# Performance work log

Hardware: AMD Instinct MI355X
Metric: run time of the kernel (lower is better)

The kernel has to match this reference:

```python
import jax, jax.numpy as jnp
import numpy as np

BATCH = 256
B_TYPES = 32   # input capsule types
C_TYPES = 10   # output capsule types
H, W = 8, 8    # input spatial extent == kernel (output is 1x1)
POSE = 16      # capsule pose length (shape (16,1))
NUM_ITER = 3
EPS = 1e-8


def setup_inputs() -> dict:
    key = jax.random.key(0)
    k1, k2, k3 = jax.random.split(key, 3)
    input_caps_poses = jax.random.normal(k1, (BATCH, B_TYPES, H, W, POSE, 1), jnp.float32)
    input_caps_activations = jax.random.uniform(k2, (BATCH, B_TYPES, H, W), jnp.float32)
    # nn.init.normal_(std=0.1) on [B, kh, kw, C, os0, is0]
    weight = 0.1 * jax.random.normal(k3, (B_TYPES, H, W, C_TYPES, POSE, POSE), jnp.float32)
    # routing_bias initialized to 0.1: [C, oh, ow, os0, os1]
    routing_bias = jnp.full((C_TYPES, 1, 1, POSE, 1), 0.1, jnp.float32)
    return {
        "input_caps_poses": input_caps_poses,
        "input_caps_activations": input_caps_activations,
        "weight": weight,
        "routing_bias": routing_bias,
    }


def _squash(s):
    # Hinton squash: ||s||^2/(1+||s||^2) * s/||s||, norm over pose dims
    n2 = jnp.sum(s * s, axis=(-2, -1), keepdims=True)
    return (n2 / (1.0 + n2)) * s * jax.lax.rsqrt(n2 + EPS)


def reference(input_caps_poses, input_caps_activations, weight, routing_bias):
    b = input_caps_poses.shape[0]
    # votes[b,c,B,h,w,o,p] = sum_i W[B,h,w,c,o,i] * pose[b,B,h,w,i,p]
    votes = jnp.einsum('Bhwcoi,bBhwip->bcBhwop', weight, input_caps_poses)
    logits = jnp.zeros((b, C_TYPES, B_TYPES, H, W), votes.dtype)
    bias = routing_bias.reshape(1, C_TYPES, POSE, 1)
    v = None
    for it in range(NUM_ITER):
        # coupling coefficients: softmax over output capsule types
        c = jax.nn.softmax(logits, axis=1)                      # [b,C,B,h,w]
        # weighted sum of votes over all input capsules (B,h,w)
        s = jnp.einsum('bcBhw,bcBhwop->bcop', c, votes) + bias  # [b,C,16,1]
        v = _squash(s)
        if it < NUM_ITER - 1:
            # agreement: dot(vote, output pose)
            logits = logits + jnp.einsum('bcBhwop,bcop->bcBhw', votes, v)
    output_caps_poses = v[:, :, None, None, :, :]               # [b,C,1,1,16,1]
    output_caps_activations = jnp.sqrt(
        jnp.sum(v * v, axis=(-2, -1)) + EPS)[:, :, None, None]  # [b,C,1,1]
    return output_caps_poses, output_caps_activations
```

## Files before the change

### kernel.cpp

```cpp
#include <hip/hip_runtime.h>
#include <hip/hip_fp16.h>
#include <math.h>


typedef _Float16 f16;
typedef _Float16 f16x2 __attribute__((ext_vector_type(2)));
typedef _Float16 f16x4 __attribute__((ext_vector_type(4)));
typedef __fp16   h16x2 __attribute__((ext_vector_type(2)));
typedef float f32x4 __attribute__((ext_vector_type(4)));

__device__ __forceinline__ f16x2 pk(float a, float b) {
    h16x2 t = __builtin_amdgcn_cvt_pkrtz(a, b);
    return __builtin_bit_cast(f16x2, t);
}

#if __has_builtin(__builtin_amdgcn_fdot2)
__device__ __forceinline__ float FDOT2(f16x2 a, f16x2 b, float c) {
    return __builtin_amdgcn_fdot2(__builtin_bit_cast(h16x2, a),
                                  __builtin_bit_cast(h16x2, b), c, false);
}
#else
__device__ __forceinline__ float FDOT2(f16x2 a, f16x2 b, float c) {
    return c + (float)a[0] * (float)b[0] + (float)a[1] * (float)b[1];
}
#endif

constexpr int WS_ROW = 28;
constexpr int XS_ROW = 76;

__device__ __forceinline__ float xorsum4(float v) {
    v += __shfl_xor(v, 16, 64);
    v += __shfl_xor(v, 32, 64);
    return v;
}

__device__ __forceinline__ f16x2 xorsum4h(f16x2 v) {
    union { f16x2 h; int i; } u;
    union { int i; f16x2 h; } w;
    u.h = v; w.i = __shfl_xor(u.i, 16, 64); v = v + w.h;
    u.h = v; w.i = __shfl_xor(u.i, 32, 64); v = v + w.h;
    return v;
}

__device__ __forceinline__ f16x4 cvt4(float4 w) {
    f16x2 a = pk(w.x, w.y);
    f16x2 b = pk(w.z, w.w);
    f16x4 r; r[0] = a[0]; r[1] = a[1]; r[2] = b[0]; r[3] = b[1];
    return r;
}

template<int PASS>
__global__ __launch_bounds__(256, 2)
void pass_k(const float* __restrict__ poses, const float* __restrict__ weight,
            const float* __restrict__ bias,
            const float* __restrict__ sp0, const float* __restrict__ sp1,
            float* __restrict__ s_dst)
{
    __shared__ f16 Ws[640 * WS_ROW];
    __shared__ f16 xs[64 * XS_ROW];

    const int tid  = threadIdx.x;
    const int blk  = blockIdx.x;
    const int ngrp = blk >> 2;
    const int b0   = (blk & 3) * 64;
    const int wave = tid >> 6;
    const int lane = tid & 63;
    const int q    = lane >> 4;
    const int lo   = lane & 15;
    const int wtb  = wave * 16;
    const int bg   = b0 + wtb;

    f16x2 vsp[10][2];
    if (PASS >= 1) {
        const int rowb = (bg + lo) * 10;
        #pragma unroll
        for (int c = 0; c < 10; ++c) {
            float4 bb = *(const float4*)(bias + c * 16 + q * 4);
            float4 sa = *(const float4*)(sp0 + (size_t)(rowb + c) * 16 + q * 4);
            float t0 = sa.x + bb.x, t1 = sa.y + bb.y, t2 = sa.z + bb.z, t3 = sa.w + bb.w;
            float n2 = xorsum4(t0*t0 + t1*t1 + t2*t2 + t3*t3);
            float sc = n2 / (1.f + n2) * rsqrtf(n2 + 1e-8f);
            float v0 = sc*t0, v1 = sc*t1, v2 = sc*t2, v3 = sc*t3;
            if (PASS == 2) {
                float4 sb = *(const float4*)(sp1 + (size_t)(rowb + c) * 16 + q * 4);
                float u0 = sb.x + bb.x, u1 = sb.y + bb.y, u2 = sb.z + bb.z, u3 = sb.w + bb.w;
                float m2 = xorsum4(u0*u0 + u1*u1 + u2*u2 + u3*u3);
                float sc2 = m2 / (1.f + m2) * rsqrtf(m2 + 1e-8f);
                v0 += sc2*u0; v1 += sc2*u1; v2 += sc2*u2; v3 += sc2*u3;
            }
            vsp[c][0] = pk(v0, v1);
            vsp[c][1] = pk(v2, v3);
        }
    }

    float4 wreg[10];
    float4 xreg[4];
    const int b_loc = tid >> 2, part = tid & 3;

    auto load_iter = [&](int l) {
        const float* wp = weight + (size_t)(ngrp * 4 + l) * 10240;
        #pragma unroll
        for (int k = 0; k < 10; ++k) wreg[k] = ((const float4*)wp)[tid + k * 256];
        const float* xp = poses + (size_t)(b0 + b_loc) * 32768
                          + (size_t)(ngrp * 16 + l * 4 + part) * 16;
        #pragma unroll
        for (int j = 0; j < 4; ++j) xreg[j] = ((const float4*)xp)[j];
    };
    auto store_iter = [&]() {
        #pragma unroll
        for (int k = 0; k < 10; ++k) {
            const int f = tid + k * 256;
            *(f16x4*)&Ws[(f >> 2) * WS_ROW + (f & 3) * 4] = cvt4(wreg[k]);
        }
        f16* lp = xs + b_loc * XS_ROW + part * 16;
        #pragma unroll
        for (int j = 0; j < 4; ++j) *(f16x4*)&lp[j * 4] = cvt4(xreg[j]);
    };

    f32x4 acc[10];
    #pragma unroll
    for (int c = 0; c < 10; ++c) acc[c] = (f32x4){0.f, 0.f, 0.f, 0.f};

    load_iter(0);

    for (int l = 0; l < 4; ++l) {
        __syncthreads();
        store_iter();
        if (l + 1 < 4) load_iter(l + 1);
        __syncthreads();

        #pragma unroll
        for (int n = 0; n < 4; ++n) {
            f16x4 bx = *(const f16x4*)&xs[(wtb + lo) * XS_ROW + n * 16 + q * 4];
            f16x2 Vh[10][2];
            #pragma unroll
            for (int c = 0; c < 10; ++c) {
                f16x4 aw = *(const f16x4*)&Ws[((n * 10 + c) * 16 + lo) * WS_ROW + q * 4];
                f32x4 V = __builtin_amdgcn_mfma_f32_16x16x16f16(
                    aw, bx, (f32x4){0.f, 0.f, 0.f, 0.f}, 0, 0, 0);
                Vh[c][0] = pk(V[0], V[1]);
                Vh[c][1] = pk(V[2], V[3]);
            }

            float cfv[10];
            if (PASS >= 1) {
                float lg[10];
                #pragma unroll
                for (int cp = 0; cp < 5; ++cp) {
                    const int c0 = cp * 2, c1 = cp * 2 + 1;
                    float p0 = FDOT2(Vh[c0][0], vsp[c0][0], 0.f);
                    p0 = FDOT2(Vh[c0][1], vsp[c0][1], p0);
                    float p1 = FDOT2(Vh[c1][0], vsp[c1][0], 0.f);
                    p1 = FDOT2(Vh[c1][1], vsp[c1][1], p1);
                    f16x2 pr = xorsum4h(pk(p0, p1));
                    lg[c0] = (float)pr[0];
                    lg[c1] = (float)pr[1];
                }
                float m = lg[0];
                #pragma unroll
                for (int c = 1; c < 10; ++c) m = fmaxf(m, lg[c]);
                float sum = 0.f;
                #pragma unroll
                for (int c = 0; c < 10; ++c) { lg[c] = __expf(lg[c] - m); sum += lg[c]; }
                const float inv = 1.f / sum;
                #pragma unroll
                for (int c = 0; c < 10; ++c) cfv[c] = lg[c] * inv;
            }

            #pragma unroll
            for (int c = 0; c < 10; ++c) {
                const float w = (PASS == 0) ? 1.f : cfv[c];
                acc[c][0] = fmaf(w, (float)Vh[c][0][0], acc[c][0]);
                acc[c][1] = fmaf(w, (float)Vh[c][0][1], acc[c][1]);
                acc[c][2] = fmaf(w, (float)Vh[c][1][0], acc[c][2]);
                acc[c][3] = fmaf(w, (float)Vh[c][1][1], acc[c][3]);
            }
        }
    }

    __syncthreads();
    float* tr = (float*)Ws + wave * 320;
    const float fs = (PASS == 0) ? 0.1f : 1.f;
    #pragma unroll
    for (int c = 0; c < 10; ++c) {
        *(float4*)&tr[lo * 20 + q * 4] = (float4){acc[c][0], acc[c][1], acc[c][2], acc[c][3]};
        float r0 = tr[(q * 4 + 0) * 20 + lo];
        float r1 = tr[(q * 4 + 1) * 20 + lo];
        float r2 = tr[(q * 4 + 2) * 20 + lo];
        float r3 = tr[(q * 4 + 3) * 20 + lo];
        float* sp = s_dst + ((size_t)(bg + q * 4) * 10 + c) * 16 + lo;
        unsafeAtomicAdd(sp + 0 * 160, fs * r0);
        unsafeAtomicAdd(sp + 1 * 160, fs * r1);
        unsafeAtomicAdd(sp + 2 * 160, fs * r2);
        unsafeAtomicAdd(sp + 3 * 160, fs * r3);
    }
}

__global__ __launch_bounds__(256)
void epi_k(const float* __restrict__ s2, const float* __restrict__ bias,
           float* __restrict__ out)
{
    const int t = blockIdx.x * 256 + threadIdx.x;
    if (t >= 2560) return;
    const int c = t % 10;
    const float* sp = s2 + (size_t)t * 16;
    const float* bp = bias + c * 16;
    float sv[16];
    float n2 = 0.f;
    #pragma unroll
    for (int o = 0; o < 16; ++o) { float v = sp[o] + bp[o]; sv[o] = v; n2 += v * v; }
    const float scale = n2 / (1.f + n2) * rsqrtf(n2 + 1e-8f);
    float a2 = 0.f;
    #pragma unroll
    for (int o = 0; o < 16; ++o) {
        float v = scale * sv[o];
        out[(size_t)t * 16 + o] = v;
        a2 += v * v;
    }
    out[40960 + t] = sqrtf(a2 + 1e-8f);
}

extern "C" void kernel_launch(void* const* d_in, const int* in_sizes, int n_in,
                              void* d_out, int out_size, void* d_ws, size_t ws_size,
                              hipStream_t stream)
{
    const float* poses  = (const float*)d_in[0];
    const float* weight = (const float*)d_in[2];
    const float* bias   = (const float*)d_in[3];
    float* out = (float*)d_out;
    float* s0 = (float*)d_ws;
    float* s1 = s0 + 40960;
    float* s2 = s1 + 40960;

    (void)hipMemsetAsync(d_ws, 0, 3 * 40960 * sizeof(float), stream);

    pass_k<0><<<512, 256, 0, stream>>>(poses, weight, bias, nullptr, nullptr, s0);
    pass_k<1><<<512, 256, 0, stream>>>(poses, weight, bias, s0, nullptr, s1);
    pass_k<2><<<512, 256, 0, stream>>>(poses, weight, bias, s0, s1, s2);
    epi_k<<<10, 256, 0, stream>>>(s2, bias, out);
}
```

Measured before the change: 203.4 us.

## Split routing passes across twice as many blocks with dual atomic accumulators and swizzled LDS

Each block now handles half as many input-capsule groups (two l-iterations instead of four), so the grid doubles to 1024 blocks and occupancy is raised to 4 blocks per CU. Atomic partial sums are spread over two accumulator buffers chosen by group parity, and readers sum both buffers, to reduce atomic contention. The weight LDS tile drops its padding and uses an XOR swizzle to avoid bank conflicts while shrinking shared memory. In exchange, the work on activations is duplicated across more blocks and partial-sum reads double; when the workspace is too small, both halves alias one buffer and a 0.5 scale compensates.

```diff
diff --git a/kernel.cpp b/kernel.cpp
--- a/kernel.cpp
+++ b/kernel.cpp
@@ -25,7 +25,6 @@
 }
 #endif
 
-constexpr int WS_ROW = 28;
 constexpr int XS_ROW = 76;
 
 __device__ __forceinline__ float xorsum4(float v) {
@@ -50,13 +49,14 @@
 }
 
 template<int PASS>
-__global__ __launch_bounds__(256, 2)
+__global__ __launch_bounds__(256, 4)
 void pass_k(const float* __restrict__ poses, const float* __restrict__ weight,
             const float* __restrict__ bias,
-            const float* __restrict__ sp0, const float* __restrict__ sp1,
-            float* __restrict__ s_dst)
+            const float* __restrict__ sp0a, const float* __restrict__ sp0b,
+            const float* __restrict__ sp1a, const float* __restrict__ sp1b,
+            float* __restrict__ s_base, int dsel, float sS)
 {
-    __shared__ f16 Ws[640 * WS_ROW];
+    __shared__ f16 Ws[640 * 16];
     __shared__ f16 xs[64 * XS_ROW];
 
     const int tid  = threadIdx.x;
@@ -70,20 +70,35 @@
     const int wtb  = wave * 16;
     const int bg   = b0 + wtb;
 
+    float* s_dst = s_base + (ngrp & 1) * dsel;
+
+    const int sr  = ((lo >> 1) ^ (lo >> 3)) & 3;
+    const int xqE = ((q ^ sr) & 3) * 4;
+    const int xqO = ((q ^ sr ^ 2) & 3) * 4;
+
     f16x2 vsp[10][2];
     if (PASS >= 1) {
         const int rowb = (bg + lo) * 10;
         #pragma unroll
         for (int c = 0; c < 10; ++c) {
             float4 bb = *(const float4*)(bias + c * 16 + q * 4);
-            float4 sa = *(const float4*)(sp0 + (size_t)(rowb + c) * 16 + q * 4);
-            float t0 = sa.x + bb.x, t1 = sa.y + bb.y, t2 = sa.z + bb.z, t3 = sa.w + bb.w;
+            const size_t off = (size_t)(rowb + c) * 16 + q * 4;
+            float4 sa = *(const float4*)(sp0a + off);
+            float4 sc4 = *(const float4*)(sp0b + off);
+            float t0 = (sa.x + sc4.x) * sS + bb.x;
+            float t1 = (sa.y + sc4.y) * sS + bb.y;
+            float t2 = (sa.z + sc4.z) * sS + bb.z;
+            float t3 = (sa.w + sc4.w) * sS + bb.w;
             float n2 = xorsum4(t0*t0 + t1*t1 + t2*t2 + t3*t3);
             float sc = n2 / (1.f + n2) * rsqrtf(n2 + 1e-8f);
             float v0 = sc*t0, v1 = sc*t1, v2 = sc*t2, v3 = sc*t3;
             if (PASS == 2) {
-                float4 sb = *(const float4*)(sp1 + (size_t)(rowb + c) * 16 + q * 4);
-                float u0 = sb.x + bb.x, u1 = sb.y + bb.y, u2 = sb.z + bb.z, u3 = sb.w + bb.w;
+                float4 ua = *(const float4*)(sp1a + off);
+                float4 ub = *(const float4*)(sp1b + off);
+                float u0 = (ua.x + ub.x) * sS + bb.x;
+                float u1 = (ua.y + ub.y) * sS + bb.y;
+                float u2 = (ua.z + ub.z) * sS + bb.z;
+                float u3 = (ua.w + ub.w) * sS + bb.w;
                 float m2 = xorsum4(u0*u0 + u1*u1 + u2*u2 + u3*u3);
                 float sc2 = m2 / (1.f + m2) * rsqrtf(m2 + 1e-8f);
                 v0 += sc2*u0; v1 += sc2*u1; v2 += sc2*u2; v3 += sc2*u3;
@@ -96,13 +111,14 @@
     float4 wreg[10];
     float4 xreg[4];
     const int b_loc = tid >> 2, part = tid & 3;
+    const int wcol = (((tid & 3) ^ ((tid >> 3) ^ (tid >> 5))) & 3) * 4;
 
     auto load_iter = [&](int l) {
-        const float* wp = weight + (size_t)(ngrp * 4 + l) * 10240;
+        const float* wp = weight + (size_t)(ngrp * 2 + l) * 10240;
         #pragma unroll
         for (int k = 0; k < 10; ++k) wreg[k] = ((const float4*)wp)[tid + k * 256];
         const float* xp = poses + (size_t)(b0 + b_loc) * 32768
-                          + (size_t)(ngrp * 16 + l * 4 + part) * 16;
+                          + (size_t)(ngrp * 8 + l * 4 + part) * 16;
         #pragma unroll
         for (int j = 0; j < 4; ++j) xreg[j] = ((const float4*)xp)[j];
     };
@@ -110,7 +126,7 @@
         #pragma unroll
         for (int k = 0; k < 10; ++k) {
             const int f = tid + k * 256;
-            *(f16x4*)&Ws[(f >> 2) * WS_ROW + (f & 3) * 4] = cvt4(wreg[k]);
+            *(f16x4*)&Ws[(f >> 2) * 16 + wcol] = cvt4(wreg[k]);
         }
         f16* lp = xs + b_loc * XS_ROW + part * 16;
         #pragma unroll
@@ -123,10 +139,10 @@
 
     load_iter(0);
 
-    for (int l = 0; l < 4; ++l) {
+    for (int l = 0; l < 2; ++l) {
         __syncthreads();
         store_iter();
-        if (l + 1 < 4) load_iter(l + 1);
+        if (l + 1 < 2) load_iter(l + 1);
         __syncthreads();
 
         #pragma unroll
@@ -135,7 +151,8 @@
             f16x2 Vh[10][2];
             #pragma unroll
             for (int c = 0; c < 10; ++c) {
-                f16x4 aw = *(const f16x4*)&Ws[((n * 10 + c) * 16 + lo) * WS_ROW + q * 4];
+                f16x4 aw = *(const f16x4*)&Ws[((n * 10 + c) * 16 + lo) * 16
+                                              + ((c & 1) ? xqO : xqE)];
                 f32x4 V = __builtin_amdgcn_mfma_f32_16x16x16f16(
                     aw, bx, (f32x4){0.f, 0.f, 0.f, 0.f}, 0, 0, 0);
                 Vh[c][0] = pk(V[0], V[1]);
@@ -197,18 +214,22 @@
 }
 
 __global__ __launch_bounds__(256)
-void epi_k(const float* __restrict__ s2, const float* __restrict__ bias,
-           float* __restrict__ out)
+void epi_k(const float* __restrict__ s2a, const float* __restrict__ s2b,
+           const float* __restrict__ bias, float* __restrict__ out, float sS)
 {
     const int t = blockIdx.x * 256 + threadIdx.x;
     if (t >= 2560) return;
     const int c = t % 10;
-    const float* sp = s2 + (size_t)t * 16;
+    const float* sp = s2a + (size_t)t * 16;
+    const float* sq = s2b + (size_t)t * 16;
     const float* bp = bias + c * 16;
     float sv[16];
     float n2 = 0.f;
     #pragma unroll
-    for (int o = 0; o < 16; ++o) { float v = sp[o] + bp[o]; sv[o] = v; n2 += v * v; }
+    for (int o = 0; o < 16; ++o) {
+        float v = (sp[o] + sq[o]) * sS + bp[o];
+        sv[o] = v; n2 += v * v;
+    }
     const float scale = n2 / (1.f + n2) * rsqrtf(n2 + 1e-8f);
     float a2 = 0.f;
     #pragma unroll
@@ -228,14 +249,23 @@
     const float* weight = (const float*)d_in[2];
     const float* bias   = (const float*)d_in[3];
     float* out = (float*)d_out;
-    float* s0 = (float*)d_ws;
-    float* s1 = s0 + 40960;
-    float* s2 = s1 + 40960;
-
-    (void)hipMemsetAsync(d_ws, 0, 3 * 40960 * sizeof(float), stream);
-
-    pass_k<0><<<512, 256, 0, stream>>>(poses, weight, bias, nullptr, nullptr, s0);
-    pass_k<1><<<512, 256, 0, stream>>>(poses, weight, bias, s0, nullptr, s1);
-    pass_k<2><<<512, 256, 0, stream>>>(poses, weight, bias, s0, s1, s2);
-    epi_k<<<10, 256, 0, stream>>>(s2, bias, out);
-}
+    float* ws  = (float*)d_ws;
+
+    const bool dual  = ws_size >= (size_t)(6 * 40960 * sizeof(float));
+    const int stride = dual ? 2 * 40960 : 40960;
+    const int dsel   = dual ? 40960 : 0;
+    const float sS   = dual ? 1.f : 0.5f;
+    float* s0 = ws;
+    float* s1 = ws + (size_t)stride;
+    float* s2 = ws + (size_t)2 * stride;
+
+    (void)hipMemsetAsync(d_ws, 0, (size_t)3 * stride * sizeof(float), stream);
+
+    pass_k<0><<<1024, 256, 0, stream>>>(poses, weight, bias,
+                                        nullptr, nullptr, nullptr, nullptr, s0, dsel, sS);
+    pass_k<1><<<1024, 256, 0, stream>>>(poses, weight, bias,
+                                        s0, s0 + dsel, nullptr, nullptr, s1, dsel, sS);
+    pass_k<2><<<1024, 256, 0, stream>>>(poses, weight, bias,
+                                        s0, s0 + dsel, s1, s1 + dsel, s2, dsel, sS);
+    epi_k<<<10, 256, 0, stream>>>(s2, s2 + dsel, bias, out, sS);
+}
```

Result: slower. 537.8 us (+164.4%).

## Halve work per block, swizzle unpadded weight LDS, raise occupancy and regroup blocks

Applied to the files above, without the earlier changes.

Each block now handles 2 spatial positions instead of 4, and the grid doubles to 1024 blocks. The weight tile in LDS drops its row padding and uses an XOR swizzle to avoid bank conflicts, which cuts shared memory per block. Launch bounds move to 3 blocks per CU, and weight/pose values are converted to fp16 at load time so the prefetch registers are half as large. Block indices are remapped so neighbouring blocks share weight groups. The trade-off is twice as many atomic adds to the accumulation buffers and less reuse of each block's weight tile.

```diff
diff --git a/kernel.cpp b/kernel.cpp
--- a/kernel.cpp
+++ b/kernel.cpp
@@ -25,7 +25,6 @@
 }
 #endif
 
-constexpr int WS_ROW = 28;
 constexpr int XS_ROW = 76;
 
 __device__ __forceinline__ float xorsum4(float v) {
@@ -50,19 +49,19 @@
 }
 
 template<int PASS>
-__global__ __launch_bounds__(256, 2)
+__global__ __launch_bounds__(256, 3)
 void pass_k(const float* __restrict__ poses, const float* __restrict__ weight,
             const float* __restrict__ bias,
             const float* __restrict__ sp0, const float* __restrict__ sp1,
             float* __restrict__ s_dst)
 {
-    __shared__ f16 Ws[640 * WS_ROW];
+    __shared__ f16 Ws[640 * 16];
     __shared__ f16 xs[64 * XS_ROW];
 
     const int tid  = threadIdx.x;
     const int blk  = blockIdx.x;
-    const int ngrp = blk >> 2;
-    const int b0   = (blk & 3) * 64;
+    const int ngrp = ((blk >> 5) << 3) | (blk & 7);
+    const int b0   = ((blk >> 3) & 3) * 64;
     const int wave = tid >> 6;
     const int lane = tid & 63;
     const int q    = lane >> 4;
@@ -70,20 +69,27 @@
     const int wtb  = wave * 16;
     const int bg   = b0 + wtb;
 
+    const int sr  = ((lo >> 1) ^ (lo >> 3)) & 3;
+    const int xqE = ((q ^ sr) & 3) * 4;
+    const int xqO = ((q ^ sr ^ 2) & 3) * 4;
+
     f16x2 vsp[10][2];
     if (PASS >= 1) {
         const int rowb = (bg + lo) * 10;
         #pragma unroll
         for (int c = 0; c < 10; ++c) {
             float4 bb = *(const float4*)(bias + c * 16 + q * 4);
-            float4 sa = *(const float4*)(sp0 + (size_t)(rowb + c) * 16 + q * 4);
-            float t0 = sa.x + bb.x, t1 = sa.y + bb.y, t2 = sa.z + bb.z, t3 = sa.w + bb.w;
+            const size_t off = (size_t)(rowb + c) * 16 + q * 4;
+            float4 sa = *(const float4*)(sp0 + off);
+            float t0 = sa.x + bb.x, t1 = sa.y + bb.y;
+            float t2 = sa.z + bb.z, t3 = sa.w + bb.w;
             float n2 = xorsum4(t0*t0 + t1*t1 + t2*t2 + t3*t3);
             float sc = n2 / (1.f + n2) * rsqrtf(n2 + 1e-8f);
             float v0 = sc*t0, v1 = sc*t1, v2 = sc*t2, v3 = sc*t3;
             if (PASS == 2) {
-                float4 sb = *(const float4*)(sp1 + (size_t)(rowb + c) * 16 + q * 4);
-                float u0 = sb.x + bb.x, u1 = sb.y + bb.y, u2 = sb.z + bb.z, u3 = sb.w + bb.w;
+                float4 ua = *(const float4*)(sp1 + off);
+                float u0 = ua.x + bb.x, u1 = ua.y + bb.y;
+                float u2 = ua.z + bb.z, u3 = ua.w + bb.w;
                 float m2 = xorsum4(u0*u0 + u1*u1 + u2*u2 + u3*u3);
                 float sc2 = m2 / (1.f + m2) * rsqrtf(m2 + 1e-8f);
                 v0 += sc2*u0; v1 += sc2*u1; v2 += sc2*u2; v3 += sc2*u3;
@@ -93,28 +99,35 @@
         }
     }
 
-    float4 wreg[10];
-    float4 xreg[4];
+    f16x4 wregh[10];
+    f16x4 xregh[4];
     const int b_loc = tid >> 2, part = tid & 3;
+    const int wcol = (((tid & 3) ^ ((tid >> 3) ^ (tid >> 5))) & 3) * 4;
 
     auto load_iter = [&](int l) {
-        const float* wp = weight + (size_t)(ngrp * 4 + l) * 10240;
-        #pragma unroll
-        for (int k = 0; k < 10; ++k) wreg[k] = ((const float4*)wp)[tid + k * 256];
+        const float* wp = weight + (size_t)(ngrp * 2 + l) * 10240;
+        #pragma unroll
+        for (int k = 0; k < 10; ++k) {
+            float4 t = ((const float4*)wp)[tid + k * 256];
+            wregh[k] = cvt4(t);
+        }
         const float* xp = poses + (size_t)(b0 + b_loc) * 32768
-                          + (size_t)(ngrp * 16 + l * 4 + part) * 16;
-        #pragma unroll
-        for (int j = 0; j < 4; ++j) xreg[j] = ((const float4*)xp)[j];
+                          + (size_t)(ngrp * 8 + l * 4 + part) * 16;
+        #pragma unroll
+        for (int j = 0; j < 4; ++j) {
+            float4 t = ((const float4*)xp)[j];
+            xregh[j] = cvt4(t);
+        }
     };
     auto store_iter = [&]() {
         #pragma unroll
         for (int k = 0; k < 10; ++k) {
             const int f = tid + k * 256;
-            *(f16x4*)&Ws[(f >> 2) * WS_ROW + (f & 3) * 4] = cvt4(wreg[k]);
+            *(f16x4*)&Ws[(f >> 2) * 16 + wcol] = wregh[k];
         }
         f16* lp = xs + b_loc * XS_ROW + part * 16;
         #pragma unroll
-        for (int j = 0; j < 4; ++j) *(f16x4*)&lp[j * 4] = cvt4(xreg[j]);
+        for (int j = 0; j < 4; ++j) *(f16x4*)&lp[j * 4] = xregh[j];
     };
 
     f32x4 acc[10];
@@ -123,10 +136,10 @@
 
     load_iter(0);
 
-    for (int l = 0; l < 4; ++l) {
+    for (int l = 0; l < 2; ++l) {
         __syncthreads();
         store_iter();
-        if (l + 1 < 4) load_iter(l + 1);
+        if (l + 1 < 2) load_iter(l + 1);
         __syncthreads();
 
         #pragma unroll
@@ -135,7 +148,8 @@
             f16x2 Vh[10][2];
             #pragma unroll
             for (int c = 0; c < 10; ++c) {
-                f16x4 aw = *(const f16x4*)&Ws[((n * 10 + c) * 16 + lo) * WS_ROW + q * 4];
+                f16x4 aw = *(const f16x4*)&Ws[((n * 10 + c) * 16 + lo) * 16
+                                              + ((c & 1) ? xqO : xqE)];
                 f32x4 V = __builtin_amdgcn_mfma_f32_16x16x16f16(
                     aw, bx, (f32x4){0.f, 0.f, 0.f, 0.f}, 0, 0, 0);
                 Vh[c][0] = pk(V[0], V[1]);
@@ -234,8 +248,8 @@
 
     (void)hipMemsetAsync(d_ws, 0, 3 * 40960 * sizeof(float), stream);
 
-    pass_k<0><<<512, 256, 0, stream>>>(poses, weight, bias, nullptr, nullptr, s0);
-    pass_k<1><<<512, 256, 0, stream>>>(poses, weight, bias, s0, nullptr, s1);
-    pass_k<2><<<512, 256, 0, stream>>>(poses, weight, bias, s0, s1, s2);
+    pass_k<0><<<1024, 256, 0, stream>>>(poses, weight, bias, nullptr, nullptr, s0);
+    pass_k<1><<<1024, 256, 0, stream>>>(poses, weight, bias, s0, nullptr, s1);
+    pass_k<2><<<1024, 256, 0, stream>>>(poses, weight, bias, s0, s1, s2);
     epi_k<<<10, 256, 0, stream>>>(s2, bias, out);
 }
```

Result: slower. 340.9 us (+67.6%).

## Load weight MFMA fragments directly from global into registers, drop LDS weight staging

Applied to the files above, without the earlier changes.

Each lane now reads its A-operand weight fragment for all 10 output types straight from global memory into registers and converts it to fp16, prefetching the next position while computing the current one. The shared-memory weight tile and the per-iteration barriers go away. All 16 positions of the pose tile are staged once into LDS up front. Launch bounds drop to one block per SM for register headroom, which lowers occupancy and exposes each wave more directly to global load latency.

```diff
diff --git a/kernel.cpp b/kernel.cpp
--- a/kernel.cpp
+++ b/kernel.cpp
@@ -25,8 +25,7 @@
 }
 #endif
 
-constexpr int WS_ROW = 28;
-constexpr int XS_ROW = 76;
+constexpr int XR = 268;
 
 __device__ __forceinline__ float xorsum4(float v) {
     v += __shfl_xor(v, 16, 64);
@@ -50,14 +49,13 @@
 }
 
 template<int PASS>
-__global__ __launch_bounds__(256, 2)
+__global__ __launch_bounds__(256, 1)
 void pass_k(const float* __restrict__ poses, const float* __restrict__ weight,
             const float* __restrict__ bias,
             const float* __restrict__ sp0, const float* __restrict__ sp1,
             float* __restrict__ s_dst)
 {
-    __shared__ f16 Ws[640 * WS_ROW];
-    __shared__ f16 xs[64 * XS_ROW];
+    __shared__ f16 xs[64 * XR];
 
     const int tid  = threadIdx.x;
     const int blk  = blockIdx.x;
@@ -69,6 +67,32 @@
     const int lo   = lane & 15;
     const int wtb  = wave * 16;
     const int bg   = b0 + wtb;
+
+    const float* wfrag = weight + (size_t)ngrp * 40960 + lo * 16 + q * 4;
+    float4 wreg[10];
+    auto load_wn = [&](int n) {
+        #pragma unroll
+        for (int c = 0; c < 10; ++c)
+            wreg[c] = *(const float4*)(wfrag + (size_t)(n * 10 + c) * 256);
+    };
+
+    load_wn(0);
+
+    const int b_loc = tid >> 2, part = tid & 3;
+    {
+        const float* xp = poses + (size_t)(b0 + b_loc) * 32768
+                          + (size_t)ngrp * 256 + part * 64;
+        float4 xr0[8], xr1[8];
+        #pragma unroll
+        for (int j = 0; j < 8; ++j) xr0[j] = ((const float4*)xp)[j];
+        #pragma unroll
+        for (int j = 0; j < 8; ++j) xr1[j] = ((const float4*)xp)[8 + j];
+        f16* lp = xs + b_loc * XR + part * 64;
+        #pragma unroll
+        for (int j = 0; j < 8; ++j) *(f16x4*)&lp[j * 4] = cvt4(xr0[j]);
+        #pragma unroll
+        for (int j = 0; j < 8; ++j) *(f16x4*)&lp[32 + j * 4] = cvt4(xr1[j]);
+    }
 
     f16x2 vsp[10][2];
     if (PASS >= 1) {
@@ -93,101 +117,73 @@
         }
     }
 
-    float4 wreg[10];
-    float4 xreg[4];
-    const int b_loc = tid >> 2, part = tid & 3;
-
-    auto load_iter = [&](int l) {
-        const float* wp = weight + (size_t)(ngrp * 4 + l) * 10240;
-        #pragma unroll
-        for (int k = 0; k < 10; ++k) wreg[k] = ((const float4*)wp)[tid + k * 256];
-        const float* xp = poses + (size_t)(b0 + b_loc) * 32768
-                          + (size_t)(ngrp * 16 + l * 4 + part) * 16;
-        #pragma unroll
-        for (int j = 0; j < 4; ++j) xreg[j] = ((const float4*)xp)[j];
-    };
-    auto store_iter = [&]() {
-        #pragma unroll
-        for (int k = 0; k < 10; ++k) {
-            const int f = tid + k * 256;
-            *(f16x4*)&Ws[(f >> 2) * WS_ROW + (f & 3) * 4] = cvt4(wreg[k]);
-        }
-        f16* lp = xs + b_loc * XS_ROW + part * 16;
-        #pragma unroll
-        for (int j = 0; j < 4; ++j) *(f16x4*)&lp[j * 4] = cvt4(xreg[j]);
-    };
-
     f32x4 acc[10];
     #pragma unroll
     for (int c = 0; c < 10; ++c) acc[c] = (f32x4){0.f, 0.f, 0.f, 0.f};
 
-    load_iter(0);
-
-    for (int l = 0; l < 4; ++l) {
-        __syncthreads();
-        store_iter();
-        if (l + 1 < 4) load_iter(l + 1);
-        __syncthreads();
-
-        #pragma unroll
-        for (int n = 0; n < 4; ++n) {
-            f16x4 bx = *(const f16x4*)&xs[(wtb + lo) * XS_ROW + n * 16 + q * 4];
-            f16x2 Vh[10][2];
-            #pragma unroll
-            for (int c = 0; c < 10; ++c) {
-                f16x4 aw = *(const f16x4*)&Ws[((n * 10 + c) * 16 + lo) * WS_ROW + q * 4];
-                f32x4 V = __builtin_amdgcn_mfma_f32_16x16x16f16(
-                    aw, bx, (f32x4){0.f, 0.f, 0.f, 0.f}, 0, 0, 0);
-                Vh[c][0] = pk(V[0], V[1]);
-                Vh[c][1] = pk(V[2], V[3]);
+    __syncthreads();
+
+    #pragma unroll 2
+    for (int n = 0; n < 16; ++n) {
+        f16x4 awh[10];
+        #pragma unroll
+        for (int c = 0; c < 10; ++c) awh[c] = cvt4(wreg[c]);
+        if (n < 15) load_wn(n + 1);
+
+        f16x4 bx = *(const f16x4*)&xs[(wtb + lo) * XR + n * 16 + q * 4];
+        f16x2 Vh[10][2];
+        #pragma unroll
+        for (int c = 0; c < 10; ++c) {
+            f32x4 V = __builtin_amdgcn_mfma_f32_16x16x16f16(
+                awh[c], bx, (f32x4){0.f, 0.f, 0.f, 0.f}, 0, 0, 0);
+            Vh[c][0] = pk(V[0], V[1]);
+            Vh[c][1] = pk(V[2], V[3]);
+        }
+
+        float cfv[10];
+        if (PASS >= 1) {
+            float lg[10];
+            #pragma unroll
+            for (int cp = 0; cp < 5; ++cp) {
+                const int c0 = cp * 2, c1 = cp * 2 + 1;
+                float p0 = FDOT2(Vh[c0][0], vsp[c0][0], 0.f);
+                p0 = FDOT2(Vh[c0][1], vsp[c0][1], p0);
+                float p1 = FDOT2(Vh[c1][0], vsp[c1][0], 0.f);
+                p1 = FDOT2(Vh[c1][1], vsp[c1][1], p1);
+                f16x2 pr = xorsum4h(pk(p0, p1));
+                lg[c0] = (float)pr[0];
+                lg[c1] = (float)pr[1];
             }
-
-            float cfv[10];
-            if (PASS >= 1) {
-                float lg[10];
-                #pragma unroll
-                for (int cp = 0; cp < 5; ++cp) {
-                    const int c0 = cp * 2, c1 = cp * 2 + 1;
-                    float p0 = FDOT2(Vh[c0][0], vsp[c0][0], 0.f);
-                    p0 = FDOT2(Vh[c0][1], vsp[c0][1], p0);
-                    float p1 = FDOT2(Vh[c1][0], vsp[c1][0], 0.f);
-                    p1 = FDOT2(Vh[c1][1], vsp[c1][1], p1);
-                    f16x2 pr = xorsum4h(pk(p0, p1));
-                    lg[c0] = (float)pr[0];
-                    lg[c1] = (float)pr[1];
-                }
-                float m = lg[0];
-                #pragma unroll
-                for (int c = 1; c < 10; ++c) m = fmaxf(m, lg[c]);
-                float sum = 0.f;
-                #pragma unroll
-                for (int c = 0; c < 10; ++c) { lg[c] = __expf(lg[c] - m); sum += lg[c]; }
-                const float inv = 1.f / sum;
-                #pragma unroll
-                for (int c = 0; c < 10; ++c) cfv[c] = lg[c] * inv;
-            }
-
-            #pragma unroll
-            for (int c = 0; c < 10; ++c) {
-                const float w = (PASS == 0) ? 1.f : cfv[c];
-                acc[c][0] = fmaf(w, (float)Vh[c][0][0], acc[c][0]);
-                acc[c][1] = fmaf(w, (float)Vh[c][0][1], acc[c][1]);
-                acc[c][2] = fmaf(w, (float)Vh[c][1][0], acc[c][2]);
-                acc[c][3] = fmaf(w, (float)Vh[c][1][1], acc[c][3]);
-            }
-        }
-    }
-
-    __syncthreads();
-    float* tr = (float*)Ws + wave * 320;
+            float m = lg[0];
+            #pragma unroll
+            for (int c = 1; c < 10; ++c) m = fmaxf(m, lg[c]);
+            float sum = 0.f;
+            #pragma unroll
+            for (int c = 0; c < 10; ++c) { lg[c] = __expf(lg[c] - m); sum += lg[c]; }
+            const float inv = 1.f / sum;
+            #pragma unroll
+            for (int c = 0; c < 10; ++c) cfv[c] = lg[c] * inv;
+        }
+
+        #pragma unroll
+        for (int c = 0; c < 10; ++c) {
+            const float w = (PASS == 0) ? 1.f : cfv[c];
+            acc[c][0] = fmaf(w, (float)Vh[c][0][0], acc[c][0]);
+            acc[c][1] = fmaf(w, (float)Vh[c][0][1], acc[c][1]);
+            acc[c][2] = fmaf(w, (float)Vh[c][1][0], acc[c][2]);
+            acc[c][3] = fmaf(w, (float)Vh[c][1][1], acc[c][3]);
+        }
+    }
+
+    float* trw = (float*)&xs[(size_t)wtb * XR];
     const float fs = (PASS == 0) ? 0.1f : 1.f;
     #pragma unroll
     for (int c = 0; c < 10; ++c) {
-        *(float4*)&tr[lo * 20 + q * 4] = (float4){acc[c][0], acc[c][1], acc[c][2], acc[c][3]};
-        float r0 = tr[(q * 4 + 0) * 20 + lo];
-        float r1 = tr[(q * 4 + 1) * 20 + lo];
-        float r2 = tr[(q * 4 + 2) * 20 + lo];
-        float r3 = tr[(q * 4 + 3) * 20 + lo];
+        *(float4*)&trw[lo * 20 + q * 4] = (float4){acc[c][0], acc[c][1], acc[c][2], acc[c][3]};
+        float r0 = trw[(q * 4 + 0) * 20 + lo];
+        float r1 = trw[(q * 4 + 1) * 20 + lo];
+        float r2 = trw[(q * 4 + 2) * 20 + lo];
+        float r3 = trw[(q * 4 + 3) * 20 + lo];
         float* sp = s_dst + ((size_t)(bg + q * 4) * 10 + c) * 16 + lo;
         unsafeAtomicAdd(sp + 0 * 160, fs * r0);
         unsafeAtomicAdd(sp + 1 * 160, fs * r1);
```

New measurement: 213.1 us. +4.7%, slower.
